# Kernel optimization log

Measured on AMD Instinct MI355X. Metric: run time of the kernel, lower is better.

The kernel has to match this reference:

```python
import jax, jax.numpy as jnp
import numpy as np

NUM_HEADS = 32
KV_HEADS = 8
HEAD_DIM = 128
HIDDEN = 4096
Q_DIM = NUM_HEADS * HEAD_DIM      # 4096
KV_DIM = KV_HEADS * HEAD_DIM      # 1024
GROUP = NUM_HEADS // KV_HEADS     # 4 (GQA)
ROPE_THETA = 10000.0
LORA_SCALE = 0.5
BP, S = 4, 1024                   # prefill requests x prefill seq len
BD, L = 64, 2048                  # decode requests x cached kv len
R, NA = 16, 8                     # lora rank, num adapters


def _rope(x, pos):
    # x: [..., n_heads, HEAD_DIM]; pos broadcastable over the token dims of x
    half = x.shape[-1] // 2
    inv = 1.0 / (ROPE_THETA ** (jnp.arange(half, dtype=jnp.float32) / half))
    freqs = pos[..., None].astype(jnp.float32) * inv          # pos.shape + (half,)
    cos = jnp.cos(freqs)[..., None, :]                        # insert head axis
    sin = jnp.sin(freqs)[..., None, :]
    x1, x2 = x[..., :half], x[..., half:]
    return jnp.concatenate([x1 * cos - x2 * sin, x2 * cos + x1 * sin], axis=-1)


def _lora(x, A, B, idx):
    # grouped multi-adapter LoRA: per-request adapter selection
    # x: [b, ..., H]; A: [NA, H, R]; B: [NA, R, D]; idx: [b]
    t = jnp.einsum('b...h,bhr->b...r', x, A[idx])
    return LORA_SCALE * jnp.einsum('b...r,brd->b...d', t, B[idx])


def setup_inputs() -> dict:
    key = jax.random.key(0)
    ks = jax.random.split(key, 16)
    T = BP * S + BD
    w = lambda k, shp: (jax.random.normal(k, shp, jnp.float32) * 0.02)
    return {
        'hidden_states': jax.random.normal(ks[0], (T, HIDDEN), jnp.float32),
        'w_qkv': w(ks[1], (HIDDEN, Q_DIM + 2 * KV_DIM)),
        'w_o': w(ks[2], (Q_DIM, HIDDEN)),
        'k_cache': jax.random.normal(ks[3], (BD, L, KV_HEADS, HEAD_DIM), jnp.float32),
        'v_cache': jax.random.normal(ks[4], (BD, L, KV_HEADS, HEAD_DIM), jnp.float32),
        'lora_a_q': w(ks[5], (NA, HIDDEN, R)),
        'lora_b_q': w(ks[6], (NA, R, Q_DIM)),
        'lora_a_k': w(ks[7], (NA, HIDDEN, R)),
        'lora_b_k': w(ks[8], (NA, R, KV_DIM)),
        'lora_a_v': w(ks[9], (NA, HIDDEN, R)),
        'lora_b_v': w(ks[10], (NA, R, KV_DIM)),
        'lora_a_o': w(ks[11], (NA, Q_DIM, R)),
        'lora_b_o': w(ks[12], (NA, R, HIDDEN)),
        'prefill_adapter_idx': jax.random.randint(ks[13], (BP,), 0, NA),
        'decode_adapter_idx': jax.random.randint(ks[14], (BD,), 0, NA),
    }


def reference(hidden_states, w_qkv, w_o, k_cache, v_cache,
              lora_a_q, lora_b_q, lora_a_k, lora_b_k, lora_a_v, lora_b_v,
              lora_a_o, lora_b_o, prefill_adapter_idx, decode_adapter_idx):
    TP = BP * S
    qkv = hidden_states @ w_qkv
    q, k, v = jnp.split(qkv, [Q_DIM, Q_DIM + KV_DIM], axis=1)

    x_p = hidden_states[:TP].reshape(BP, S, HIDDEN)
    x_d = hidden_states[TP:]

    # apply_lora_weight_kvq: per-request adapters on q/k/v
    q_p = q[:TP].reshape(BP, S, Q_DIM) + _lora(x_p, lora_a_q, lora_b_q, prefill_adapter_idx)
    k_p = k[:TP].reshape(BP, S, KV_DIM) + _lora(x_p, lora_a_k, lora_b_k, prefill_adapter_idx)
    v_p = v[:TP].reshape(BP, S, KV_DIM) + _lora(x_p, lora_a_v, lora_b_v, prefill_adapter_idx)
    q_d = q[TP:] + _lora(x_d, lora_a_q, lora_b_q, decode_adapter_idx)
    k_d = k[TP:] + _lora(x_d, lora_a_k, lora_b_k, decode_adapter_idx)
    v_d = v[TP:] + _lora(x_d, lora_a_v, lora_b_v, decode_adapter_idx)

    scale = 1.0 / np.sqrt(HEAD_DIM).astype(np.float32)

    # ---- prefill: causal self-attention with on-the-fly RoPE ----
    q_p = _rope(q_p.reshape(BP, S, NUM_HEADS, HEAD_DIM), jnp.arange(S, dtype=jnp.float32))
    k_p = _rope(k_p.reshape(BP, S, KV_HEADS, HEAD_DIM), jnp.arange(S, dtype=jnp.float32))
    v_p = v_p.reshape(BP, S, KV_HEADS, HEAD_DIM)
    kr = jnp.repeat(k_p, GROUP, axis=2)
    vr = jnp.repeat(v_p, GROUP, axis=2)
    scores = jnp.einsum('bqhd,bkhd->bhqk', q_p, kr) * scale
    causal = jnp.tril(jnp.ones((S, S), bool))
    scores = jnp.where(causal, scores, -jnp.inf)
    attn = jax.nn.softmax(scores, axis=-1)
    out_p = jnp.einsum('bhqk,bkhd->bqhd', attn, vr).reshape(TP, Q_DIM)

    # ---- decode: one new token per request vs paged KV cache ----
    q_d = _rope(q_d.reshape(BD, NUM_HEADS, HEAD_DIM), jnp.asarray(L, jnp.float32))
    k_new = _rope(k_d.reshape(BD, KV_HEADS, HEAD_DIM), jnp.asarray(L, jnp.float32))
    k_hist = _rope(k_cache, jnp.arange(L, dtype=jnp.float32))
    k_all = jnp.concatenate([k_hist, k_new[:, None]], axis=1)   # [BD, L+1, kvh, hd]
    v_all = jnp.concatenate([v_cache, v_d.reshape(BD, 1, KV_HEADS, HEAD_DIM)], axis=1)
    kr2 = jnp.repeat(k_all, GROUP, axis=2)
    vr2 = jnp.repeat(v_all, GROUP, axis=2)
    s2 = jnp.einsum('bhd,bkhd->bhk', q_d, kr2) * scale
    a2 = jax.nn.softmax(s2, axis=-1)
    out_d = jnp.einsum('bhk,bkhd->bhd', a2, vr2).reshape(BD, Q_DIM)

    # ---- o_proj + apply_lora_weight_attn ----
    attn_raw = jnp.concatenate([out_p, out_d], axis=0)
    o = attn_raw @ w_o
    o_p = o[:TP].reshape(BP, S, HIDDEN) + _lora(attn_raw[:TP].reshape(BP, S, Q_DIM), lora_a_o, lora_b_o, prefill_adapter_idx)
    o_d = o[TP:] + _lora(attn_raw[TP:], lora_a_o, lora_b_o, decode_adapter_idx)
    return jnp.concatenate([o_p.reshape(TP, HIDDEN), o_d], axis=0)
```

## Files before the change

### kernel.cpp

```cpp
#include <hip/hip_runtime.h>

#define NUM_HEADS 32
#define KV_HEADS 8
#define HEAD_DIM 128
#define HIDDEN 4096
#define Q_DIM 4096
#define KV_DIM 1024
#define QKV_DIM 6144
#define GROUP 4
#define BP 4
#define S_LEN 1024
#define BD 64
#define L_CTX 2048
#define RANK 16
#define NA 8
#define TP (BP * S_LEN)
#define T_TOT (TP + BD)
#define M_PAD 4224
#define SCALE 0.08838834764831845f
#define LORA_SCALE 0.5f
#define DNSPLIT 16
#define DSPLIT_LEN 128
#define DP_STRIDE 520

typedef float fv4 __attribute__((ext_vector_type(4)));
typedef __bf16 bf16x8 __attribute__((ext_vector_type(8)));
typedef unsigned short usv4 __attribute__((ext_vector_type(4)));
typedef unsigned short u16;

__device__ __forceinline__ float b2f(u16 u) {
    unsigned int x = ((unsigned int)u) << 16;
    return __builtin_bit_cast(float, x);
}
__device__ __forceinline__ u16 f2b(float f) {
    unsigned int u = __builtin_bit_cast(unsigned int, f);
    unsigned int r = u + 0x7fffu + ((u >> 16) & 1u);
    return (u16)(r >> 16);
}
__device__ __forceinline__ void gload_lds16(const void* g, void* l) {
    __builtin_amdgcn_global_load_lds((const __attribute__((address_space(1))) void*)g,
                                     (__attribute__((address_space(3))) void*)l, 16, 0, 0);
}
__device__ __forceinline__ float dot16(const float* __restrict__ a, const float* __restrict__ b) {
    float s = 0.f;
#pragma unroll
    for (int q = 0; q < 4; ++q) {
        fv4 av = *(const fv4*)(a + q * 4);
        fv4 bv = *(const fv4*)(b + q * 4);
        s += av[0] * bv[0] + av[1] * bv[1] + av[2] * bv[2] + av[3] * bv[3];
    }
    return s;
}

#define OFF_QKV  ((size_t)0)
#define OFF_ATTN OFF_QKV
#define OFF_HB   ((size_t)51904512)
#define OFF_QP   OFF_HB
#define OFF_WOT  OFF_HB
#define OFF_WQT  ((size_t)86507520)
#define OFF_KP   ((size_t)86507520)
#define OFF_VP   ((size_t)94896128)
#define OFF_QD   ((size_t)103284736)
#define OFF_KD   ((size_t)104333312)
#define OFF_VD   ((size_t)104595456)
#define OFF_DP   ((size_t)104857600)
#define OFF_BQT  ((size_t)121896960)
#define OFF_BKT  ((size_t)123994112)
#define OFF_BVT  ((size_t)124518400)
#define OFF_BOT  ((size_t)125042688)
#define OFF_T    ((size_t)136839168)
#define OFF_TO   ((size_t)137637888)
#define OFF_COS  ((size_t)137904128)
#define OFF_SIN  ((size_t)138428672)

__global__ void rope_tab_kernel(float* ctab, float* stab) {
    int idx = blockIdx.x * 256 + threadIdx.x;
    if (idx >= 2049 * 64) return;
    int pos = idx >> 6, d = idx & 63;
    float inv = 1.0f / powf(10000.0f, (float)d / 64.0f);
    float f = (float)pos * inv;
    ctab[idx] = cosf(f);
    stab[idx] = sinf(f);
}

__global__ void conv_hidden_kernel(const float* __restrict__ x, u16* __restrict__ y) {
    int gid = blockIdx.x * 256 + threadIdx.x;
    if (gid >= M_PAD * (HIDDEN / 8)) return;
    size_t base = (size_t)gid * 8;
    int row = gid >> 9;
    usv4 lo, hi;
    if (row < T_TOT) {
        fv4 a = *(const fv4*)(x + base);
        fv4 b = *(const fv4*)(x + base + 4);
        lo[0] = f2b(a[0]); lo[1] = f2b(a[1]); lo[2] = f2b(a[2]); lo[3] = f2b(a[3]);
        hi[0] = f2b(b[0]); hi[1] = f2b(b[1]); hi[2] = f2b(b[2]); hi[3] = f2b(b[3]);
    } else {
        lo[0] = 0; lo[1] = 0; lo[2] = 0; lo[3] = 0;
        hi[0] = 0; hi[1] = 0; hi[2] = 0; hi[3] = 0;
    }
    *(usv4*)(y + base) = lo;
    *(usv4*)(y + base + 4) = hi;
}

__global__ __launch_bounds__(256) void transpose_f32_bf16_kernel(const float* __restrict__ in,
                                                                 u16* __restrict__ out,
                                                                 int R, int C) {
    __shared__ float tile[64][65];
    int r0 = blockIdx.y * 64, c0 = blockIdx.x * 64;
    int t = threadIdx.x;
    int tr = t >> 4, tc4 = (t & 15) * 4;
#pragma unroll
    for (int it = 0; it < 4; ++it) {
        int r = tr + it * 16;
        fv4 v = *(const fv4*)(in + (size_t)(r0 + r) * C + c0 + tc4);
        tile[r][tc4 + 0] = v[0]; tile[r][tc4 + 1] = v[1];
        tile[r][tc4 + 2] = v[2]; tile[r][tc4 + 3] = v[3];
    }
    __syncthreads();
#pragma unroll
    for (int it = 0; it < 4; ++it) {
        int c = tr + it * 16;
        usv4 st;
        st[0] = f2b(tile[tc4 + 0][c]); st[1] = f2b(tile[tc4 + 1][c]);
        st[2] = f2b(tile[tc4 + 2][c]); st[3] = f2b(tile[tc4 + 3][c]);
        *(usv4*)(out + (size_t)(c0 + c) * R + r0 + tc4) = st;
    }
}

__global__ void btrans_kernel(const float* __restrict__ Bq, const float* __restrict__ Bk,
                              const float* __restrict__ Bv, const float* __restrict__ Bo,
                              float* __restrict__ BqT, float* __restrict__ BkT,
                              float* __restrict__ BvT, float* __restrict__ BoT) {
    int gid = blockIdx.x * 256 + threadIdx.x;
    const int NQ = NA * 4096 * 16;
    const int NK = NA * 1024 * 16;
    if (gid < NQ) {
        int a = gid >> 16, rem = gid & 65535, c = rem >> 4, r = rem & 15;
        BqT[gid] = Bq[((size_t)(a * 16 + r)) * 4096 + c];
    } else if (gid < NQ + NK) {
        int g = gid - NQ;
        int a = g >> 14, rem = g & 16383, c = rem >> 4, r = rem & 15;
        BkT[g] = Bk[((size_t)(a * 16 + r)) * 1024 + c];
    } else if (gid < NQ + 2 * NK) {
        int g = gid - NQ - NK;
        int a = g >> 14, rem = g & 16383, c = rem >> 4, r = rem & 15;
        BvT[g] = Bv[((size_t)(a * 16 + r)) * 1024 + c];
    } else if (gid < 2 * NQ + 2 * NK) {
        int g = gid - NQ - 2 * NK;
        int a = g >> 16, rem = g & 65535, c = rem >> 4, r = rem & 15;
        BoT[g] = Bo[((size_t)(a * 16 + r)) * 4096 + c];
    }
}

__global__ __launch_bounds__(256) void lora_a_kernel(const float* __restrict__ x,
                              const float* __restrict__ Aq, const float* __restrict__ Ak,
                              const float* __restrict__ Av,
                              const int* __restrict__ pidx, const int* __restrict__ didx,
                              float* __restrict__ T) {
    __shared__ float xs[4][HIDDEN];
    int t0 = blockIdx.x * 4;
    int tid = threadIdx.x;
    for (int j = tid; j < 4096; j += 256) {
        int tok = j >> 10, off = (j & 1023) * 4;
        *(fv4*)&xs[tok][off] = *(const fv4*)(x + (size_t)(t0 + tok) * HIDDEN + off);
    }
    __syncthreads();
    int w = tid >> 6, lane = tid & 63;
    if (w >= 3) return;
    const float* Ab = (w == 0) ? Aq : (w == 1 ? Ak : Av);
    float acc[4][16];
#pragma unroll
    for (int tk = 0; tk < 4; ++tk)
#pragma unroll
        for (int r = 0; r < 16; ++r) acc[tk][r] = 0.f;
#pragma unroll
    for (int tk = 0; tk < 4; ++tk) {
        int t = t0 + tk;
        int a = (t < TP) ? pidx[t >> 10] : didx[t - TP];
        const float* A = Ab + (size_t)a * HIDDEN * RANK;
        for (int i = 0; i < 64; ++i) {
            int hh = i * 64 + lane;
            float xv = xs[tk][hh];
            const float* Ar = A + (size_t)hh * RANK;
            fv4 a0 = *(const fv4*)Ar, a1 = *(const fv4*)(Ar + 4);
            fv4 a2 = *(const fv4*)(Ar + 8), a3 = *(const fv4*)(Ar + 12);
#pragma unroll
            for (int r = 0; r < 4; ++r) {
                acc[tk][r] += xv * a0[r];
                acc[tk][4 + r] += xv * a1[r];
                acc[tk][8 + r] += xv * a2[r];
                acc[tk][12 + r] += xv * a3[r];
            }
        }
    }
#pragma unroll
    for (int tk = 0; tk < 4; ++tk)
#pragma unroll
        for (int r = 0; r < 16; ++r) {
            float v = acc[tk][r];
            v += __shfl_xor(v, 1); v += __shfl_xor(v, 2); v += __shfl_xor(v, 4);
            v += __shfl_xor(v, 8); v += __shfl_xor(v, 16); v += __shfl_xor(v, 32);
            if (lane == r) T[(size_t)(t0 + tk) * 48 + w * 16 + r] = v;
        }
}

template <int OUT_BF16>
__global__ __launch_bounds__(256) void gemm_bt_kernel(const u16* __restrict__ A,
                                                      const u16* __restrict__ BT,
                                                      void* __restrict__ Cp,
                                                      int Mstore, int N, int K) {
    __shared__ __align__(16) u16 As[2][128 * 32];
    __shared__ __align__(16) u16 Bs[2][128 * 32];
    int tid = threadIdx.x;
    int m0 = blockIdx.y * 128, n0 = blockIdx.x * 128;
    int lane = tid & 63, w = tid >> 6, lr = lane & 15, lg = lane >> 4;
    int wr = w >> 1, wc = w & 1;
    int arow = tid >> 2, acol = (tid & 3) * 8;
    const u16* Ab = A + (size_t)(m0 + arow) * K + acol;
    const u16* Bb = BT + (size_t)(n0 + arow) * K + acol;
    fv4 acc[4][4] = {};
    int nt = K / 32;
#define GSTAGE(buf, kk)                                                             \
    {                                                                               \
        char* Ad = (char*)&As[buf][0] + w * 1024;                                   \
        char* Bd = (char*)&Bs[buf][0] + w * 1024;                                   \
        gload_lds16(Ab + (kk), Ad);                                                 \
        gload_lds16(Ab + (size_t)64 * K + (kk), Ad + 4096);                         \
        gload_lds16(Bb + (kk), Bd);                                                 \
        gload_lds16(Bb + (size_t)64 * K + (kk), Bd + 4096);                         \
    }
    GSTAGE(0, 0)
    __syncthreads();
    int cur = 0;
    for (int t = 0; t < nt; ++t) {
        if (t + 1 < nt) GSTAGE(cur ^ 1, (t + 1) * 32)
        bf16x8 af[4], bf[4];
#pragma unroll
        for (int i = 0; i < 4; ++i) {
            af[i] = *(const bf16x8*)&As[cur][(wr * 64 + i * 16 + lr) * 32 + lg * 8];
            bf[i] = *(const bf16x8*)&Bs[cur][(wc * 64 + i * 16 + lr) * 32 + lg * 8];
        }
#pragma unroll
        for (int mi = 0; mi < 4; ++mi)
#pragma unroll
            for (int ni = 0; ni < 4; ++ni)
                acc[mi][ni] = __builtin_amdgcn_mfma_f32_16x16x32_bf16(af[mi], bf[ni], acc[mi][ni], 0, 0, 0);
        __syncthreads();
        cur ^= 1;
    }
#undef GSTAGE
#pragma unroll
    for (int mi = 0; mi < 4; ++mi)
#pragma unroll
        for (int ni = 0; ni < 4; ++ni) {
            int col = n0 + wc * 64 + ni * 16 + lr;
#pragma unroll
            for (int r = 0; r < 4; ++r) {
                int row = m0 + wr * 64 + mi * 16 + lg * 4 + r;
                if (row < Mstore) {
                    if (OUT_BF16)
                        ((u16*)Cp)[(size_t)row * N + col] = f2b(acc[mi][ni][r]);
                    else
                        ((float*)Cp)[(size_t)row * N + col] = acc[mi][ni][r];
                }
            }
        }
}

__global__ __launch_bounds__(256) void lorab_rope_scatter_kernel(
    const u16* __restrict__ qkv, const float* __restrict__ T,
    const float* __restrict__ BqT, const float* __restrict__ BkT, const float* __restrict__ BvT,
    const int* __restrict__ pidx, const int* __restrict__ didx,
    const float* __restrict__ ctab, const float* __restrict__ stab,
    u16* __restrict__ qp, u16* __restrict__ kp, u16* __restrict__ vp,
    float* __restrict__ qd, float* __restrict__ kd, float* __restrict__ vd) {
    int t = blockIdx.x;
    __shared__ __align__(16) float Ts[48];
    if (threadIdx.x < 48) Ts[threadIdx.x] = T[(size_t)t * 48 + threadIdx.x];
    __syncthreads();
    bool pre = t < TP;
    int a = pre ? pidx[t >> 10] : didx[t - TP];
    int pos = pre ? (t & 1023) : L_CTX;
    int b = t >> 10;
    int td = t - TP;
    const u16* qrow = qkv + (size_t)t * QKV_DIM;
    for (int p = threadIdx.x; p < 3072; p += 256) {
        if (p < 2048) {
            int h = p >> 6, d = p & 63;
            int col = h * 128 + d;
            float v1 = b2f(qrow[col]), v2 = b2f(qrow[col + 64]);
            const float* B1 = BqT + ((size_t)(a * 4096 + col)) * 16;
            const float* B2 = BqT + ((size_t)(a * 4096 + col + 64)) * 16;
            float l1 = dot16(&Ts[0], B1);
            float l2 = dot16(&Ts[0], B2);
            v1 += LORA_SCALE * l1; v2 += LORA_SCALE * l2;
            float c = ctab[pos * 64 + d], s = stab[pos * 64 + d];
            float o1 = v1 * c - v2 * s, o2 = v2 * c + v1 * s;
            if (pre) {
                size_t base = (((size_t)(b * 32 + h)) * 1024 + pos) * 128 + d;
                qp[base] = f2b(o1); qp[base + 64] = f2b(o2);
            } else {
                size_t base = ((size_t)(td * 32 + h)) * 128 + d;
                qd[base] = o1; qd[base + 64] = o2;
            }
        } else if (p < 2560) {
            int pp = p - 2048;
            int h = pp >> 6, d = pp & 63;
            int jc = h * 128 + d;
            int col = Q_DIM + jc;
            float v1 = b2f(qrow[col]), v2 = b2f(qrow[col + 64]);
            const float* B1 = BkT + ((size_t)(a * 1024 + jc)) * 16;
            const float* B2 = BkT + ((size_t)(a * 1024 + jc + 64)) * 16;
            float l1 = dot16(&Ts[16], B1);
            float l2 = dot16(&Ts[16], B2);
            v1 += LORA_SCALE * l1; v2 += LORA_SCALE * l2;
            float c = ctab[pos * 64 + d], s = stab[pos * 64 + d];
            float o1 = v1 * c - v2 * s, o2 = v2 * c + v1 * s;
            if (pre) {
                size_t base = (((size_t)(b * 8 + h)) * 1024 + pos) * 128 + d;
                kp[base] = f2b(o1); kp[base + 64] = f2b(o2);
            } else {
                size_t base = ((size_t)(td * 8 + h)) * 128 + d;
                kd[base] = o1; kd[base + 64] = o2;
            }
        } else {
            int pp = p - 2560;
            int h = pp >> 6, d = pp & 63;
            int jc = h * 128 + d;
            int col = Q_DIM + KV_DIM + jc;
            float v1 = b2f(qrow[col]), v2 = b2f(qrow[col + 64]);
            const float* B1 = BvT + ((size_t)(a * 1024 + jc)) * 16;
            const float* B2 = BvT + ((size_t)(a * 1024 + jc + 64)) * 16;
            float l1 = dot16(&Ts[32], B1);
            float l2 = dot16(&Ts[32], B2);
            v1 += LORA_SCALE * l1; v2 += LORA_SCALE * l2;
            if (pre) {
                size_t base = (((size_t)(b * 8 + h)) * 1024 + pos) * 128 + d;
                vp[base] = f2b(v1); vp[base + 64] = f2b(v2);
            } else {
                size_t base = ((size_t)(td * 8 + h)) * 128 + d;
                vd[base] = v1; vd[base + 64] = v2;
            }
        }
    }
}

__global__ __launch_bounds__(256) void prefill_attn_kernel(const u16* __restrict__ qp,
                                                           const u16* __restrict__ kp,
                                                           const u16* __restrict__ vp,
                                                           u16* __restrict__ attn) {
    int bx = blockIdx.x;
    int qt = (bx & 1) ? (31 - (bx >> 1)) : (bx >> 1);
    int kvh = blockIdx.y, b = blockIdx.z;
    int tid = threadIdx.x, w = tid >> 6, lane = tid & 63, lr = lane & 15, lg = lane >> 4;
    int h = kvh * 4 + w;
    const u16* Q = qp + ((size_t)(b * 32 + h)) * 1024 * 128;
    const u16* K = kp + ((size_t)(b * 8 + kvh)) * 1024 * 128;
    const u16* V = vp + ((size_t)(b * 8 + kvh)) * 1024 * 128;
    int qc0 = qt * 32 + lr, qc1 = qt * 32 + 16 + lr;
    bf16x8 qf0[4], qf1[4];
#pragma unroll
    for (int dc = 0; dc < 4; ++dc) {
        qf0[dc] = *(const bf16x8*)(Q + (size_t)qc0 * 128 + dc * 32 + lg * 8);
        qf1[dc] = *(const bf16x8*)(Q + (size_t)qc1 * 128 + dc * 32 + lg * 8);
    }
    fv4 o0[8] = {}, o1[8] = {};
    float m0 = -INFINITY, l0 = 0.f;
    float m1 = -INFINITY, l1 = 0.f;
    int nkb = qt + 1;
    for (int kb = 0; kb < nkb; ++kb) {
        int k0 = kb * 32;
        fv4 s00 = {}, s10 = {}, s01 = {}, s11 = {};
#pragma unroll
        for (int dc = 0; dc < 4; ++dc) {
            bf16x8 kf0 = *(const bf16x8*)(K + (size_t)(k0 + lr) * 128 + dc * 32 + lg * 8);
            bf16x8 kf1 = *(const bf16x8*)(K + (size_t)(k0 + 16 + lr) * 128 + dc * 32 + lg * 8);
            s00 = __builtin_amdgcn_mfma_f32_16x16x32_bf16(kf0, qf0[dc], s00, 0, 0, 0);
            s10 = __builtin_amdgcn_mfma_f32_16x16x32_bf16(kf1, qf0[dc], s10, 0, 0, 0);
            s01 = __builtin_amdgcn_mfma_f32_16x16x32_bf16(kf0, qf1[dc], s01, 0, 0, 0);
            s11 = __builtin_amdgcn_mfma_f32_16x16x32_bf16(kf1, qf1[dc], s11, 0, 0, 0);
        }
        bf16x8 vf[8];
#pragma unroll
        for (int c = 0; c < 8; ++c)
#pragma unroll
            for (int i = 0; i < 4; ++i) {
                vf[c][i] = __builtin_bit_cast(__bf16, V[(size_t)(k0 + lg * 4 + i) * 128 + c * 16 + lr]);
                vf[c][4 + i] = __builtin_bit_cast(__bf16, V[(size_t)(k0 + 16 + lg * 4 + i) * 128 + c * 16 + lr]);
            }
        bf16x8 pf0, pf1;
        {
            float p0[4], p1[4];
            float lm = -INFINITY;
#pragma unroll
            for (int r = 0; r < 4; ++r) {
                float x = s00[r] * SCALE;
                if (k0 + lg * 4 + r > qc0) x = -INFINITY;
                p0[r] = x; lm = fmaxf(lm, x);
                x = s10[r] * SCALE;
                if (k0 + 16 + lg * 4 + r > qc0) x = -INFINITY;
                p1[r] = x; lm = fmaxf(lm, x);
            }
            lm = fmaxf(lm, __shfl_xor(lm, 16));
            lm = fmaxf(lm, __shfl_xor(lm, 32));
            float mn = fmaxf(m0, lm);
            float sc = __expf(m0 - mn);
            float rs = 0.f;
#pragma unroll
            for (int r = 0; r < 4; ++r) {
                p0[r] = __expf(p0[r] - mn);
                p1[r] = __expf(p1[r] - mn);
                rs += p0[r] + p1[r];
            }
            rs += __shfl_xor(rs, 16);
            rs += __shfl_xor(rs, 32);
            l0 = l0 * sc + rs;
            m0 = mn;
#pragma unroll
            for (int c = 0; c < 8; ++c) o0[c] *= sc;
#pragma unroll
            for (int r = 0; r < 4; ++r) {
                pf0[r] = (__bf16)p0[r];
                pf0[4 + r] = (__bf16)p1[r];
            }
        }
        {
            float p0[4], p1[4];
            float lm = -INFINITY;
#pragma unroll
            for (int r = 0; r < 4; ++r) {
                float x = s01[r] * SCALE;
                if (k0 + lg * 4 + r > qc1) x = -INFINITY;
                p0[r] = x; lm = fmaxf(lm, x);
                x = s11[r] * SCALE;
                if (k0 + 16 + lg * 4 + r > qc1) x = -INFINITY;
                p1[r] = x; lm = fmaxf(lm, x);
            }
            lm = fmaxf(lm, __shfl_xor(lm, 16));
            lm = fmaxf(lm, __shfl_xor(lm, 32));
            float mn = fmaxf(m1, lm);
            float sc = __expf(m1 - mn);
            float rs = 0.f;
#pragma unroll
            for (int r = 0; r < 4; ++r) {
                p0[r] = __expf(p0[r] - mn);
                p1[r] = __expf(p1[r] - mn);
                rs += p0[r] + p1[r];
            }
            rs += __shfl_xor(rs, 16);
            rs += __shfl_xor(rs, 32);
            l1 = l1 * sc + rs;
            m1 = mn;
#pragma unroll
            for (int c = 0; c < 8; ++c) o1[c] *= sc;
#pragma unroll
            for (int r = 0; r < 4; ++r) {
                pf1[r] = (__bf16)p0[r];
                pf1[4 + r] = (__bf16)p1[r];
            }
        }
#pragma unroll
        for (int c = 0; c < 8; ++c) {
            o0[c] = __builtin_amdgcn_mfma_f32_16x16x32_bf16(vf[c], pf0, o0[c], 0, 0, 0);
            o1[c] = __builtin_amdgcn_mfma_f32_16x16x32_bf16(vf[c], pf1, o1[c], 0, 0, 0);
        }
    }
    float inv0 = 1.0f / l0, inv1 = 1.0f / l1;
    size_t trow0 = (size_t)(b * 1024 + qc0) * Q_DIM;
    size_t trow1 = (size_t)(b * 1024 + qc1) * Q_DIM;
#pragma unroll
    for (int c = 0; c < 8; ++c)
#pragma unroll
        for (int r = 0; r < 4; ++r) {
            int feat = h * 128 + c * 16 + lg * 4 + r;
            attn[trow0 + feat] = f2b(o0[c][r] * inv0);
            attn[trow1 + feat] = f2b(o1[c][r] * inv1);
        }
}

template <int FIRST_HALF>
__device__ __forceinline__ bf16x8 krope8(const float* __restrict__ Krow,
                                         const float* __restrict__ ct,
                                         const float* __restrict__ st, int d0) {
    bf16x8 out;
    if (FIRST_HALF) {
        fv4 a0 = *(const fv4*)(Krow + d0), a1 = *(const fv4*)(Krow + d0 + 4);
        fv4 b0 = *(const fv4*)(Krow + d0 + 64), b1 = *(const fv4*)(Krow + d0 + 68);
        fv4 c0 = *(const fv4*)(ct + d0), c1 = *(const fv4*)(ct + d0 + 4);
        fv4 s0 = *(const fv4*)(st + d0), s1 = *(const fv4*)(st + d0 + 4);
#pragma unroll
        for (int i = 0; i < 4; ++i) {
            out[i] = (__bf16)(a0[i] * c0[i] - b0[i] * s0[i]);
            out[4 + i] = (__bf16)(a1[i] * c1[i] - b1[i] * s1[i]);
        }
    } else {
        int dd = d0 - 64;
        fv4 a0 = *(const fv4*)(Krow + d0), a1 = *(const fv4*)(Krow + d0 + 4);
        fv4 b0 = *(const fv4*)(Krow + dd), b1 = *(const fv4*)(Krow + dd + 4);
        fv4 c0 = *(const fv4*)(ct + dd), c1 = *(const fv4*)(ct + dd + 4);
        fv4 s0 = *(const fv4*)(st + dd), s1 = *(const fv4*)(st + dd + 4);
#pragma unroll
        for (int i = 0; i < 4; ++i) {
            out[i] = (__bf16)(a0[i] * c0[i] + b0[i] * s0[i]);
            out[4 + i] = (__bf16)(a1[i] * c1[i] + b1[i] * s1[i]);
        }
    }
    return out;
}

__global__ __launch_bounds__(128) void decode_attn_kernel(const float* __restrict__ kc,
                                                          const float* __restrict__ vc,
                                                          const float* __restrict__ qd,
                                                          const float* __restrict__ ctab,
                                                          const float* __restrict__ stab,
                                                          float* __restrict__ dp) {
    int blk = blockIdx.x;
    int bk = blk >> 3;
    int b = bk >> 3, kvh = bk & 7;
    int wv = threadIdx.x >> 6, lane = threadIdx.x & 63;
    int s = (blk & 7) * 2 + wv;
    int lr = lane & 15, lg = lane >> 4;
    const float* Qrow = qd + ((size_t)(b * 32 + kvh * 4 + (lr & 3))) * 128;
    bf16x8 qf[4];
#pragma unroll
    for (int dc = 0; dc < 4; ++dc) {
        int d0 = dc * 32 + lg * 8;
        fv4 q0 = *(const fv4*)(Qrow + d0), q1 = *(const fv4*)(Qrow + d0 + 4);
#pragma unroll
        for (int i = 0; i < 4; ++i) {
            qf[dc][i] = (__bf16)q0[i];
            qf[dc][4 + i] = (__bf16)q1[i];
        }
    }
    fv4 o[8] = {};
    float m = -INFINITY, l = 0.f;
    int kbase = s * DSPLIT_LEN;
    for (int t = 0; t < 4; ++t) {
        int k0 = kbase + t * 32;
        int key0 = k0 + lr, key1 = k0 + 16 + lr;
        const float* K0 = kc + (((size_t)b * L_CTX + key0) * 8 + kvh) * 128;
        const float* K1 = kc + (((size_t)b * L_CTX + key1) * 8 + kvh) * 128;
        const float* ct0 = ctab + key0 * 64;
        const float* st0 = stab + key0 * 64;
        const float* ct1 = ctab + key1 * 64;
        const float* st1 = stab + key1 * 64;
        fv4 s0 = {}, s1 = {};
#pragma unroll
        for (int dc = 0; dc < 4; ++dc) {
            int d0 = dc * 32 + lg * 8;
            bf16x8 kf0, kf1;
            if (dc < 2) {
                kf0 = krope8<1>(K0, ct0, st0, d0);
                kf1 = krope8<1>(K1, ct1, st1, d0);
            } else {
                kf0 = krope8<0>(K0, ct0, st0, d0);
                kf1 = krope8<0>(K1, ct1, st1, d0);
            }
            s0 = __builtin_amdgcn_mfma_f32_16x16x32_bf16(kf0, qf[dc], s0, 0, 0, 0);
            s1 = __builtin_amdgcn_mfma_f32_16x16x32_bf16(kf1, qf[dc], s1, 0, 0, 0);
        }
        const float* Vb = vc + (((size_t)b * L_CTX + k0) * 8 + kvh) * 128;
        bf16x8 vf[8];
#pragma unroll
        for (int c = 0; c < 8; ++c)
#pragma unroll
            for (int i = 0; i < 4; ++i) {
                vf[c][i] = (__bf16)Vb[(size_t)(lg * 4 + i) * 1024 + c * 16 + lr];
                vf[c][4 + i] = (__bf16)Vb[(size_t)(16 + lg * 4 + i) * 1024 + c * 16 + lr];
            }
        float p0[4], p1[4];
        float lm = -INFINITY;
#pragma unroll
        for (int r = 0; r < 4; ++r) {
            float x = s0[r] * SCALE;
            p0[r] = x; lm = fmaxf(lm, x);
            x = s1[r] * SCALE;
            p1[r] = x; lm = fmaxf(lm, x);
        }
        lm = fmaxf(lm, __shfl_xor(lm, 16));
        lm = fmaxf(lm, __shfl_xor(lm, 32));
        float mn = fmaxf(m, lm);
        float sc = __expf(m - mn);
        float rs = 0.f;
#pragma unroll
        for (int r = 0; r < 4; ++r) {
            p0[r] = __expf(p0[r] - mn);
            p1[r] = __expf(p1[r] - mn);
            rs += p0[r] + p1[r];
        }
        rs += __shfl_xor(rs, 16);
        rs += __shfl_xor(rs, 32);
        l = l * sc + rs;
        m = mn;
#pragma unroll
        for (int c = 0; c < 8; ++c) o[c] *= sc;
        bf16x8 pf;
#pragma unroll
        for (int r = 0; r < 4; ++r) {
            pf[r] = (__bf16)p0[r];
            pf[4 + r] = (__bf16)p1[r];
        }
#pragma unroll
        for (int c = 0; c < 8; ++c)
            o[c] = __builtin_amdgcn_mfma_f32_16x16x32_bf16(vf[c], pf, o[c], 0, 0, 0);
    }
    size_t base = ((size_t)(bk * DNSPLIT + s)) * DP_STRIDE;
    if (lr < 4) {
#pragma unroll
        for (int c = 0; c < 8; ++c)
#pragma unroll
            for (int r = 0; r < 4; ++r)
                dp[base + 8 + lr * 128 + c * 16 + lg * 4 + r] = o[c][r];
        if (lg == 0) { dp[base + lr] = m; dp[base + 4 + lr] = l; }
    }
}

__global__ __launch_bounds__(256) void decode_merge_kernel(const float* __restrict__ dp,
                                                           const float* __restrict__ qd,
                                                           const float* __restrict__ kd,
                                                           const float* __restrict__ vd,
                                                           u16* __restrict__ attn) {
    int bk = blockIdx.x;
    int b = bk >> 3, kvh = bk & 7;
    int g = threadIdx.x >> 6, lane = threadIdx.x & 63;
    size_t qb = ((size_t)(b * 32 + kvh * 4 + g)) * 128;
    float q1 = qd[qb + lane], q2 = qd[qb + 64 + lane];
    size_t kb = ((size_t)(b * 8 + kvh)) * 128;
    float k1 = kd[kb + lane], k2 = kd[kb + 64 + lane];
    float v1 = vd[kb + lane], v2 = vd[kb + 64 + lane];
    float part = q1 * k1 + q2 * k2;
#pragma unroll
    for (int off = 32; off; off >>= 1) part += __shfl_xor(part, off);
    float snew = part * SCALE;
    float M = snew;
#pragma unroll
    for (int s = 0; s < DNSPLIT; ++s)
        M = fmaxf(M, dp[((size_t)(bk * DNSPLIT + s)) * DP_STRIDE + g]);
    float L = 0.f, O1 = 0.f, O2 = 0.f;
#pragma unroll
    for (int s = 0; s < DNSPLIT; ++s) {
        size_t base = ((size_t)(bk * DNSPLIT + s)) * DP_STRIDE;
        float e = __expf(dp[base + g] - M);
        L += dp[base + 4 + g] * e;
        O1 += dp[base + 8 + g * 128 + lane] * e;
        O2 += dp[base + 8 + g * 128 + 64 + lane] * e;
    }
    float en = __expf(snew - M);
    L += en; O1 += en * v1; O2 += en * v2;
    size_t orow = (size_t)(TP + b) * Q_DIM + (kvh * 4 + g) * 128;
    attn[orow + lane] = f2b(O1 / L);
    attn[orow + 64 + lane] = f2b(O2 / L);
}

__global__ __launch_bounds__(64) void lora_o_a_kernel(const u16* __restrict__ attn,
                                const float* __restrict__ Ao,
                                const int* __restrict__ pidx, const int* __restrict__ didx,
                                float* __restrict__ To) {
    __shared__ float xs[4][HIDDEN];
    int t0 = blockIdx.x * 4;
    int lane = threadIdx.x;
    for (int j = lane; j < 4096; j += 64) {
        int tok = j >> 10, off = (j & 1023) * 4;
        usv4 v = *(const usv4*)(attn + (size_t)(t0 + tok) * Q_DIM + off);
        xs[tok][off] = b2f(v[0]); xs[tok][off + 1] = b2f(v[1]);
        xs[tok][off + 2] = b2f(v[2]); xs[tok][off + 3] = b2f(v[3]);
    }
    __syncthreads();
    float acc[4][16];
#pragma unroll
    for (int tk = 0; tk < 4; ++tk)
#pragma unroll
        for (int r = 0; r < 16; ++r) acc[tk][r] = 0.f;
#pragma unroll
    for (int tk = 0; tk < 4; ++tk) {
        int t = t0 + tk;
        int a = (t < TP) ? pidx[t >> 10] : didx[t - TP];
        const float* A = Ao + (size_t)a * Q_DIM * RANK;
        for (int i = 0; i < 64; ++i) {
            int hh = i * 64 + lane;
            float xv = xs[tk][hh];
            const float* Ar = A + (size_t)hh * RANK;
            fv4 a0 = *(const fv4*)Ar, a1 = *(const fv4*)(Ar + 4);
            fv4 a2 = *(const fv4*)(Ar + 8), a3 = *(const fv4*)(Ar + 12);
#pragma unroll
            for (int r = 0; r < 4; ++r) {
                acc[tk][r] += xv * a0[r];
                acc[tk][4 + r] += xv * a1[r];
                acc[tk][8 + r] += xv * a2[r];
                acc[tk][12 + r] += xv * a3[r];
            }
        }
    }
#pragma unroll
    for (int tk = 0; tk < 4; ++tk)
#pragma unroll
        for (int r = 0; r < 16; ++r) {
            float v = acc[tk][r];
            v += __shfl_xor(v, 1); v += __shfl_xor(v, 2); v += __shfl_xor(v, 4);
            v += __shfl_xor(v, 8); v += __shfl_xor(v, 16); v += __shfl_xor(v, 32);
            if (lane == r) To[(size_t)(t0 + tk) * RANK + r] = v;
        }
}

__global__ void final_lora_add_kernel(float* __restrict__ out, const float* __restrict__ To,
                                      const float* __restrict__ BoT,
                                      const int* __restrict__ pidx, const int* __restrict__ didx) {
    int gid = blockIdx.x * 256 + threadIdx.x;
    if (gid >= T_TOT * HIDDEN) return;
    int t = gid >> 12, j = gid & 4095;
    int a = (t < TP) ? pidx[t >> 10] : didx[t - TP];
    const float* B = BoT + ((size_t)(a * 4096 + j)) * 16;
    const float* Tr = To + (size_t)t * RANK;
    out[gid] += LORA_SCALE * dot16(Tr, B);
}

extern "C" void kernel_launch(void* const* d_in, const int* in_sizes, int n_in,
                              void* d_out, int out_size, void* d_ws, size_t ws_size,
                              hipStream_t stream) {
    const float* hidden = (const float*)d_in[0];
    const float* w_qkv = (const float*)d_in[1];
    const float* w_o = (const float*)d_in[2];
    const float* k_cache = (const float*)d_in[3];
    const float* v_cache = (const float*)d_in[4];
    const float* Aq = (const float*)d_in[5];
    const float* Bq = (const float*)d_in[6];
    const float* Ak = (const float*)d_in[7];
    const float* Bk = (const float*)d_in[8];
    const float* Av = (const float*)d_in[9];
    const float* Bv = (const float*)d_in[10];
    const float* Ao = (const float*)d_in[11];
    const float* Bo = (const float*)d_in[12];
    const int* pidx = (const int*)d_in[13];
    const int* didx = (const int*)d_in[14];
    float* out = (float*)d_out;

    char* ws = (char*)d_ws;
    u16* qkv = (u16*)(ws + OFF_QKV);
    u16* attn = (u16*)(ws + OFF_ATTN);
    u16* hb = (u16*)(ws + OFF_HB);
    u16* wqT = (u16*)(ws + OFF_WQT);
    u16* woT = (u16*)(ws + OFF_WOT);
    float* T = (float*)(ws + OFF_T);
    u16* qp = (u16*)(ws + OFF_QP);
    u16* kp = (u16*)(ws + OFF_KP);
    u16* vp = (u16*)(ws + OFF_VP);
    float* qd = (float*)(ws + OFF_QD);
    float* kd = (float*)(ws + OFF_KD);
    float* vd = (float*)(ws + OFF_VD);
    float* dp = (float*)(ws + OFF_DP);
    float* BqT = (float*)(ws + OFF_BQT);
    float* BkT = (float*)(ws + OFF_BKT);
    float* BvT = (float*)(ws + OFF_BVT);
    float* BoT = (float*)(ws + OFF_BOT);
    float* To = (float*)(ws + OFF_TO);
    float* ctab = (float*)(ws + OFF_COS);
    float* stab = (float*)(ws + OFF_SIN);

    rope_tab_kernel<<<513, 256, 0, stream>>>(ctab, stab);
    conv_hidden_kernel<<<(M_PAD * (HIDDEN / 8) + 255) / 256, 256, 0, stream>>>(hidden, hb);
    transpose_f32_bf16_kernel<<<dim3(QKV_DIM / 64, HIDDEN / 64), 256, 0, stream>>>(w_qkv, wqT, HIDDEN, QKV_DIM);
    lora_a_kernel<<<T_TOT / 4, 256, 0, stream>>>(hidden, Aq, Ak, Av, pidx, didx, T);
    gemm_bt_kernel<1><<<dim3(QKV_DIM / 128, M_PAD / 128), 256, 0, stream>>>(hb, wqT, qkv, M_PAD, QKV_DIM, HIDDEN);
    btrans_kernel<<<(2 * (NA * 4096 * 16) + 2 * (NA * 1024 * 16) + 255) / 256, 256, 0, stream>>>(
        Bq, Bk, Bv, Bo, BqT, BkT, BvT, BoT);
    lorab_rope_scatter_kernel<<<T_TOT, 256, 0, stream>>>(qkv, T, BqT, BkT, BvT, pidx, didx,
                                                         ctab, stab, qp, kp, vp, qd, kd, vd);
    prefill_attn_kernel<<<dim3(32, 8, 4), 256, 0, stream>>>(qp, kp, vp, attn);
    decode_attn_kernel<<<4096, 128, 0, stream>>>(k_cache, v_cache, qd, ctab, stab, dp);
    decode_merge_kernel<<<512, 256, 0, stream>>>(dp, qd, kd, vd, attn);
    transpose_f32_bf16_kernel<<<dim3(HIDDEN / 64, Q_DIM / 64), 256, 0, stream>>>(w_o, woT, Q_DIM, HIDDEN);
    lora_o_a_kernel<<<T_TOT / 4, 64, 0, stream>>>(attn, Ao, pidx, didx, To);
    gemm_bt_kernel<0><<<dim3(HIDDEN / 128, M_PAD / 128), 256, 0, stream>>>(attn, woT, out, T_TOT, HIDDEN, Q_DIM);
    final_lora_add_kernel<<<(T_TOT * HIDDEN + 255) / 256, 256, 0, stream>>>(out, To, BoT, pidx, didx);
}
```

Before: 1.633 ms.

## Fuse prefill and decode attention into one interleaved launch

Merges the prefill flash-attention kernel and the split-K decode attention kernel into a single launch of 3072 blocks. Every third block runs a prefill tile and the other two run decode splits, with decode blocks now holding 4 waves instead of 2. The aim is to overlap the memory-bound decode KV-cache streaming with the compute-heavy causal prefill and remove one launch plus its tail. The cost is higher register pressure from the union of both paths, which may lower occupancy, and a block-role branch.

New measurement: 1.695 ms. +3.8%, slower.

```diff
diff --git a/kernel.cpp b/kernel.cpp
--- a/kernel.cpp
+++ b/kernel.cpp
@@ -345,139 +345,6 @@
     }
 }
 
-__global__ __launch_bounds__(256) void prefill_attn_kernel(const u16* __restrict__ qp,
-                                                           const u16* __restrict__ kp,
-                                                           const u16* __restrict__ vp,
-                                                           u16* __restrict__ attn) {
-    int bx = blockIdx.x;
-    int qt = (bx & 1) ? (31 - (bx >> 1)) : (bx >> 1);
-    int kvh = blockIdx.y, b = blockIdx.z;
-    int tid = threadIdx.x, w = tid >> 6, lane = tid & 63, lr = lane & 15, lg = lane >> 4;
-    int h = kvh * 4 + w;
-    const u16* Q = qp + ((size_t)(b * 32 + h)) * 1024 * 128;
-    const u16* K = kp + ((size_t)(b * 8 + kvh)) * 1024 * 128;
-    const u16* V = vp + ((size_t)(b * 8 + kvh)) * 1024 * 128;
-    int qc0 = qt * 32 + lr, qc1 = qt * 32 + 16 + lr;
-    bf16x8 qf0[4], qf1[4];
-#pragma unroll
-    for (int dc = 0; dc < 4; ++dc) {
-        qf0[dc] = *(const bf16x8*)(Q + (size_t)qc0 * 128 + dc * 32 + lg * 8);
-        qf1[dc] = *(const bf16x8*)(Q + (size_t)qc1 * 128 + dc * 32 + lg * 8);
-    }
-    fv4 o0[8] = {}, o1[8] = {};
-    float m0 = -INFINITY, l0 = 0.f;
-    float m1 = -INFINITY, l1 = 0.f;
-    int nkb = qt + 1;
-    for (int kb = 0; kb < nkb; ++kb) {
-        int k0 = kb * 32;
-        fv4 s00 = {}, s10 = {}, s01 = {}, s11 = {};
-#pragma unroll
-        for (int dc = 0; dc < 4; ++dc) {
-            bf16x8 kf0 = *(const bf16x8*)(K + (size_t)(k0 + lr) * 128 + dc * 32 + lg * 8);
-            bf16x8 kf1 = *(const bf16x8*)(K + (size_t)(k0 + 16 + lr) * 128 + dc * 32 + lg * 8);
-            s00 = __builtin_amdgcn_mfma_f32_16x16x32_bf16(kf0, qf0[dc], s00, 0, 0, 0);
-            s10 = __builtin_amdgcn_mfma_f32_16x16x32_bf16(kf1, qf0[dc], s10, 0, 0, 0);
-            s01 = __builtin_amdgcn_mfma_f32_16x16x32_bf16(kf0, qf1[dc], s01, 0, 0, 0);
-            s11 = __builtin_amdgcn_mfma_f32_16x16x32_bf16(kf1, qf1[dc], s11, 0, 0, 0);
-        }
-        bf16x8 vf[8];
-#pragma unroll
-        for (int c = 0; c < 8; ++c)
-#pragma unroll
-            for (int i = 0; i < 4; ++i) {
-                vf[c][i] = __builtin_bit_cast(__bf16, V[(size_t)(k0 + lg * 4 + i) * 128 + c * 16 + lr]);
-                vf[c][4 + i] = __builtin_bit_cast(__bf16, V[(size_t)(k0 + 16 + lg * 4 + i) * 128 + c * 16 + lr]);
-            }
-        bf16x8 pf0, pf1;
-        {
-            float p0[4], p1[4];
-            float lm = -INFINITY;
-#pragma unroll
-            for (int r = 0; r < 4; ++r) {
-                float x = s00[r] * SCALE;
-                if (k0 + lg * 4 + r > qc0) x = -INFINITY;
-                p0[r] = x; lm = fmaxf(lm, x);
-                x = s10[r] * SCALE;
-                if (k0 + 16 + lg * 4 + r > qc0) x = -INFINITY;
-                p1[r] = x; lm = fmaxf(lm, x);
-            }
-            lm = fmaxf(lm, __shfl_xor(lm, 16));
-            lm = fmaxf(lm, __shfl_xor(lm, 32));
-            float mn = fmaxf(m0, lm);
-            float sc = __expf(m0 - mn);
-            float rs = 0.f;
-#pragma unroll
-            for (int r = 0; r < 4; ++r) {
-                p0[r] = __expf(p0[r] - mn);
-                p1[r] = __expf(p1[r] - mn);
-                rs += p0[r] + p1[r];
-            }
-            rs += __shfl_xor(rs, 16);
-            rs += __shfl_xor(rs, 32);
-            l0 = l0 * sc + rs;
-            m0 = mn;
-#pragma unroll
-            for (int c = 0; c < 8; ++c) o0[c] *= sc;
-#pragma unroll
-            for (int r = 0; r < 4; ++r) {
-                pf0[r] = (__bf16)p0[r];
-                pf0[4 + r] = (__bf16)p1[r];
-            }
-        }
-        {
-            float p0[4], p1[4];
-            float lm = -INFINITY;
-#pragma unroll
-            for (int r = 0; r < 4; ++r) {
-                float x = s01[r] * SCALE;
-                if (k0 + lg * 4 + r > qc1) x = -INFINITY;
-                p0[r] = x; lm = fmaxf(lm, x);
-                x = s11[r] * SCALE;
-                if (k0 + 16 + lg * 4 + r > qc1) x = -INFINITY;
-                p1[r] = x; lm = fmaxf(lm, x);
-            }
-            lm = fmaxf(lm, __shfl_xor(lm, 16));
-            lm = fmaxf(lm, __shfl_xor(lm, 32));
-            float mn = fmaxf(m1, lm);
-            float sc = __expf(m1 - mn);
-            float rs = 0.f;
-#pragma unroll
-            for (int r = 0; r < 4; ++r) {
-                p0[r] = __expf(p0[r] - mn);
-                p1[r] = __expf(p1[r] - mn);
-                rs += p0[r] + p1[r];
-            }
-            rs += __shfl_xor(rs, 16);
-            rs += __shfl_xor(rs, 32);
-            l1 = l1 * sc + rs;
-            m1 = mn;
-#pragma unroll
-            for (int c = 0; c < 8; ++c) o1[c] *= sc;
-#pragma unroll
-            for (int r = 0; r < 4; ++r) {
-                pf1[r] = (__bf16)p0[r];
-                pf1[4 + r] = (__bf16)p1[r];
-            }
-        }
-#pragma unroll
-        for (int c = 0; c < 8; ++c) {
-            o0[c] = __builtin_amdgcn_mfma_f32_16x16x32_bf16(vf[c], pf0, o0[c], 0, 0, 0);
-            o1[c] = __builtin_amdgcn_mfma_f32_16x16x32_bf16(vf[c], pf1, o1[c], 0, 0, 0);
-        }
-    }
-    float inv0 = 1.0f / l0, inv1 = 1.0f / l1;
-    size_t trow0 = (size_t)(b * 1024 + qc0) * Q_DIM;
-    size_t trow1 = (size_t)(b * 1024 + qc1) * Q_DIM;
-#pragma unroll
-    for (int c = 0; c < 8; ++c)
-#pragma unroll
-        for (int r = 0; r < 4; ++r) {
-            int feat = h * 128 + c * 16 + lg * 4 + r;
-            attn[trow0 + feat] = f2b(o0[c][r] * inv0);
-            attn[trow1 + feat] = f2b(o1[c][r] * inv1);
-        }
-}
-
 template <int FIRST_HALF>
 __device__ __forceinline__ bf16x8 krope8(const float* __restrict__ Krow,
                                          const float* __restrict__ ct,
@@ -508,110 +375,240 @@
     return out;
 }
 
-__global__ __launch_bounds__(128) void decode_attn_kernel(const float* __restrict__ kc,
-                                                          const float* __restrict__ vc,
-                                                          const float* __restrict__ qd,
-                                                          const float* __restrict__ ctab,
-                                                          const float* __restrict__ stab,
-                                                          float* __restrict__ dp) {
-    int blk = blockIdx.x;
-    int bk = blk >> 3;
-    int b = bk >> 3, kvh = bk & 7;
-    int wv = threadIdx.x >> 6, lane = threadIdx.x & 63;
-    int s = (blk & 7) * 2 + wv;
-    int lr = lane & 15, lg = lane >> 4;
-    const float* Qrow = qd + ((size_t)(b * 32 + kvh * 4 + (lr & 3))) * 128;
-    bf16x8 qf[4];
-#pragma unroll
-    for (int dc = 0; dc < 4; ++dc) {
-        int d0 = dc * 32 + lg * 8;
-        fv4 q0 = *(const fv4*)(Qrow + d0), q1 = *(const fv4*)(Qrow + d0 + 4);
-#pragma unroll
-        for (int i = 0; i < 4; ++i) {
-            qf[dc][i] = (__bf16)q0[i];
-            qf[dc][4 + i] = (__bf16)q1[i];
-        }
-    }
-    fv4 o[8] = {};
-    float m = -INFINITY, l = 0.f;
-    int kbase = s * DSPLIT_LEN;
-    for (int t = 0; t < 4; ++t) {
-        int k0 = kbase + t * 32;
-        int key0 = k0 + lr, key1 = k0 + 16 + lr;
-        const float* K0 = kc + (((size_t)b * L_CTX + key0) * 8 + kvh) * 128;
-        const float* K1 = kc + (((size_t)b * L_CTX + key1) * 8 + kvh) * 128;
-        const float* ct0 = ctab + key0 * 64;
-        const float* st0 = stab + key0 * 64;
-        const float* ct1 = ctab + key1 * 64;
-        const float* st1 = stab + key1 * 64;
-        fv4 s0 = {}, s1 = {};
+__global__ __launch_bounds__(256) void attn_fused_kernel(
+    const u16* __restrict__ qp, const u16* __restrict__ kp, const u16* __restrict__ vp,
+    u16* __restrict__ attn,
+    const float* __restrict__ kc, const float* __restrict__ vc, const float* __restrict__ qd,
+    const float* __restrict__ ctab, const float* __restrict__ stab, float* __restrict__ dp) {
+    int bid = blockIdx.x;
+    int tid = threadIdx.x, lane = tid & 63, lr = lane & 15, lg = lane >> 4;
+    if (bid % 3 == 0) {
+        int pb = bid / 3;
+        int bx = pb & 31, kvh = (pb >> 5) & 7, b = pb >> 8;
+        int qt = (bx & 1) ? (31 - (bx >> 1)) : (bx >> 1);
+        int w = tid >> 6;
+        int h = kvh * 4 + w;
+        const u16* Q = qp + ((size_t)(b * 32 + h)) * 1024 * 128;
+        const u16* K = kp + ((size_t)(b * 8 + kvh)) * 1024 * 128;
+        const u16* V = vp + ((size_t)(b * 8 + kvh)) * 1024 * 128;
+        int qc0 = qt * 32 + lr, qc1 = qt * 32 + 16 + lr;
+        bf16x8 qf0[4], qf1[4];
+#pragma unroll
+        for (int dc = 0; dc < 4; ++dc) {
+            qf0[dc] = *(const bf16x8*)(Q + (size_t)qc0 * 128 + dc * 32 + lg * 8);
+            qf1[dc] = *(const bf16x8*)(Q + (size_t)qc1 * 128 + dc * 32 + lg * 8);
+        }
+        fv4 o0[8] = {}, o1[8] = {};
+        float m0 = -INFINITY, l0 = 0.f;
+        float m1 = -INFINITY, l1 = 0.f;
+        int nkb = qt + 1;
+        for (int kb = 0; kb < nkb; ++kb) {
+            int k0 = kb * 32;
+            fv4 s00 = {}, s10 = {}, s01 = {}, s11 = {};
+#pragma unroll
+            for (int dc = 0; dc < 4; ++dc) {
+                bf16x8 kf0 = *(const bf16x8*)(K + (size_t)(k0 + lr) * 128 + dc * 32 + lg * 8);
+                bf16x8 kf1 = *(const bf16x8*)(K + (size_t)(k0 + 16 + lr) * 128 + dc * 32 + lg * 8);
+                s00 = __builtin_amdgcn_mfma_f32_16x16x32_bf16(kf0, qf0[dc], s00, 0, 0, 0);
+                s10 = __builtin_amdgcn_mfma_f32_16x16x32_bf16(kf1, qf0[dc], s10, 0, 0, 0);
+                s01 = __builtin_amdgcn_mfma_f32_16x16x32_bf16(kf0, qf1[dc], s01, 0, 0, 0);
+                s11 = __builtin_amdgcn_mfma_f32_16x16x32_bf16(kf1, qf1[dc], s11, 0, 0, 0);
+            }
+            bf16x8 vf[8];
+#pragma unroll
+            for (int c = 0; c < 8; ++c)
+#pragma unroll
+                for (int i = 0; i < 4; ++i) {
+                    vf[c][i] = __builtin_bit_cast(__bf16, V[(size_t)(k0 + lg * 4 + i) * 128 + c * 16 + lr]);
+                    vf[c][4 + i] = __builtin_bit_cast(__bf16, V[(size_t)(k0 + 16 + lg * 4 + i) * 128 + c * 16 + lr]);
+                }
+            bf16x8 pf0, pf1;
+            {
+                float p0[4], p1[4];
+                float lm = -INFINITY;
+#pragma unroll
+                for (int r = 0; r < 4; ++r) {
+                    float x = s00[r] * SCALE;
+                    if (k0 + lg * 4 + r > qc0) x = -INFINITY;
+                    p0[r] = x; lm = fmaxf(lm, x);
+                    x = s10[r] * SCALE;
+                    if (k0 + 16 + lg * 4 + r > qc0) x = -INFINITY;
+                    p1[r] = x; lm = fmaxf(lm, x);
+                }
+                lm = fmaxf(lm, __shfl_xor(lm, 16));
+                lm = fmaxf(lm, __shfl_xor(lm, 32));
+                float mn = fmaxf(m0, lm);
+                float sc = __expf(m0 - mn);
+                float rs = 0.f;
+#pragma unroll
+                for (int r = 0; r < 4; ++r) {
+                    p0[r] = __expf(p0[r] - mn);
+                    p1[r] = __expf(p1[r] - mn);
+                    rs += p0[r] + p1[r];
+                }
+                rs += __shfl_xor(rs, 16);
+                rs += __shfl_xor(rs, 32);
+                l0 = l0 * sc + rs;
+                m0 = mn;
+#pragma unroll
+                for (int c = 0; c < 8; ++c) o0[c] *= sc;
+#pragma unroll
+                for (int r = 0; r < 4; ++r) {
+                    pf0[r] = (__bf16)p0[r];
+                    pf0[4 + r] = (__bf16)p1[r];
+                }
+            }
+            {
+                float p0[4], p1[4];
+                float lm = -INFINITY;
+#pragma unroll
+                for (int r = 0; r < 4; ++r) {
+                    float x = s01[r] * SCALE;
+                    if (k0 + lg * 4 + r > qc1) x = -INFINITY;
+                    p0[r] = x; lm = fmaxf(lm, x);
+                    x = s11[r] * SCALE;
+                    if (k0 + 16 + lg * 4 + r > qc1) x = -INFINITY;
+                    p1[r] = x; lm = fmaxf(lm, x);
+                }
+                lm = fmaxf(lm, __shfl_xor(lm, 16));
+                lm = fmaxf(lm, __shfl_xor(lm, 32));
+                float mn = fmaxf(m1, lm);
+                float sc = __expf(m1 - mn);
+                float rs = 0.f;
+#pragma unroll
+                for (int r = 0; r < 4; ++r) {
+                    p0[r] = __expf(p0[r] - mn);
+                    p1[r] = __expf(p1[r] - mn);
+                    rs += p0[r] + p1[r];
+                }
+                rs += __shfl_xor(rs, 16);
+                rs += __shfl_xor(rs, 32);
+                l1 = l1 * sc + rs;
+                m1 = mn;
+#pragma unroll
+                for (int c = 0; c < 8; ++c) o1[c] *= sc;
+#pragma unroll
+                for (int r = 0; r < 4; ++r) {
+                    pf1[r] = (__bf16)p0[r];
+                    pf1[4 + r] = (__bf16)p1[r];
+                }
+            }
+#pragma unroll
+            for (int c = 0; c < 8; ++c) {
+                o0[c] = __builtin_amdgcn_mfma_f32_16x16x32_bf16(vf[c], pf0, o0[c], 0, 0, 0);
+                o1[c] = __builtin_amdgcn_mfma_f32_16x16x32_bf16(vf[c], pf1, o1[c], 0, 0, 0);
+            }
+        }
+        float inv0 = 1.0f / l0, inv1 = 1.0f / l1;
+        size_t trow0 = (size_t)(b * 1024 + qc0) * Q_DIM;
+        size_t trow1 = (size_t)(b * 1024 + qc1) * Q_DIM;
+#pragma unroll
+        for (int c = 0; c < 8; ++c)
+#pragma unroll
+            for (int r = 0; r < 4; ++r) {
+                int feat = h * 128 + c * 16 + lg * 4 + r;
+                attn[trow0 + feat] = f2b(o0[c][r] * inv0);
+                attn[trow1 + feat] = f2b(o1[c][r] * inv1);
+            }
+    } else {
+        int db = (bid / 3) * 2 + (bid % 3) - 1;
+        int bk = db >> 2;
+        int b = bk >> 3, kvh = bk & 7;
+        int wv = tid >> 6;
+        int s = (db & 3) * 4 + wv;
+        const float* Qrow = qd + ((size_t)(b * 32 + kvh * 4 + (lr & 3))) * 128;
+        bf16x8 qf[4];
 #pragma unroll
         for (int dc = 0; dc < 4; ++dc) {
             int d0 = dc * 32 + lg * 8;
-            bf16x8 kf0, kf1;
-            if (dc < 2) {
-                kf0 = krope8<1>(K0, ct0, st0, d0);
-                kf1 = krope8<1>(K1, ct1, st1, d0);
-            } else {
-                kf0 = krope8<0>(K0, ct0, st0, d0);
-                kf1 = krope8<0>(K1, ct1, st1, d0);
-            }
-            s0 = __builtin_amdgcn_mfma_f32_16x16x32_bf16(kf0, qf[dc], s0, 0, 0, 0);
-            s1 = __builtin_amdgcn_mfma_f32_16x16x32_bf16(kf1, qf[dc], s1, 0, 0, 0);
-        }
-        const float* Vb = vc + (((size_t)b * L_CTX + k0) * 8 + kvh) * 128;
-        bf16x8 vf[8];
-#pragma unroll
-        for (int c = 0; c < 8; ++c)
+            fv4 q0 = *(const fv4*)(Qrow + d0), q1 = *(const fv4*)(Qrow + d0 + 4);
 #pragma unroll
             for (int i = 0; i < 4; ++i) {
-                vf[c][i] = (__bf16)Vb[(size_t)(lg * 4 + i) * 1024 + c * 16 + lr];
-                vf[c][4 + i] = (__bf16)Vb[(size_t)(16 + lg * 4 + i) * 1024 + c * 16 + lr];
-            }
-        float p0[4], p1[4];
-        float lm = -INFINITY;
-#pragma unroll
-        for (int r = 0; r < 4; ++r) {
-            float x = s0[r] * SCALE;
-            p0[r] = x; lm = fmaxf(lm, x);
-            x = s1[r] * SCALE;
-            p1[r] = x; lm = fmaxf(lm, x);
-        }
-        lm = fmaxf(lm, __shfl_xor(lm, 16));
-        lm = fmaxf(lm, __shfl_xor(lm, 32));
-        float mn = fmaxf(m, lm);
-        float sc = __expf(m - mn);
-        float rs = 0.f;
-#pragma unroll
-        for (int r = 0; r < 4; ++r) {
-            p0[r] = __expf(p0[r] - mn);
-            p1[r] = __expf(p1[r] - mn);
-            rs += p0[r] + p1[r];
-        }
-        rs += __shfl_xor(rs, 16);
-        rs += __shfl_xor(rs, 32);
-        l = l * sc + rs;
-        m = mn;
-#pragma unroll
-        for (int c = 0; c < 8; ++c) o[c] *= sc;
-        bf16x8 pf;
-#pragma unroll
-        for (int r = 0; r < 4; ++r) {
-            pf[r] = (__bf16)p0[r];
-            pf[4 + r] = (__bf16)p1[r];
-        }
-#pragma unroll
-        for (int c = 0; c < 8; ++c)
-            o[c] = __builtin_amdgcn_mfma_f32_16x16x32_bf16(vf[c], pf, o[c], 0, 0, 0);
-    }
-    size_t base = ((size_t)(bk * DNSPLIT + s)) * DP_STRIDE;
-    if (lr < 4) {
-#pragma unroll
-        for (int c = 0; c < 8; ++c)
-#pragma unroll
-            for (int r = 0; r < 4; ++r)
-                dp[base + 8 + lr * 128 + c * 16 + lg * 4 + r] = o[c][r];
-        if (lg == 0) { dp[base + lr] = m; dp[base + 4 + lr] = l; }
+                qf[dc][i] = (__bf16)q0[i];
+                qf[dc][4 + i] = (__bf16)q1[i];
+            }
+        }
+        fv4 o[8] = {};
+        float m = -INFINITY, l = 0.f;
+        int kbase = s * DSPLIT_LEN;
+        for (int t = 0; t < 4; ++t) {
+            int k0 = kbase + t * 32;
+            int key0 = k0 + lr, key1 = k0 + 16 + lr;
+            const float* K0 = kc + (((size_t)b * L_CTX + key0) * 8 + kvh) * 128;
+            const float* K1 = kc + (((size_t)b * L_CTX + key1) * 8 + kvh) * 128;
+            const float* ct0 = ctab + key0 * 64;
+            const float* st0 = stab + key0 * 64;
+            const float* ct1 = ctab + key1 * 64;
+            const float* st1 = stab + key1 * 64;
+            fv4 s0 = {}, s1 = {};
+#pragma unroll
+            for (int dc = 0; dc < 4; ++dc) {
+                int d0 = dc * 32 + lg * 8;
+                bf16x8 kf0, kf1;
+                if (dc < 2) {
+                    kf0 = krope8<1>(K0, ct0, st0, d0);
+                    kf1 = krope8<1>(K1, ct1, st1, d0);
+                } else {
+                    kf0 = krope8<0>(K0, ct0, st0, d0);
+                    kf1 = krope8<0>(K1, ct1, st1, d0);
+                }
+                s0 = __builtin_amdgcn_mfma_f32_16x16x32_bf16(kf0, qf[dc], s0, 0, 0, 0);
+                s1 = __builtin_amdgcn_mfma_f32_16x16x32_bf16(kf1, qf[dc], s1, 0, 0, 0);
+            }
+            const float* Vb = vc + (((size_t)b * L_CTX + k0) * 8 + kvh) * 128;
+            bf16x8 vf[8];
+#pragma unroll
+            for (int c = 0; c < 8; ++c)
+#pragma unroll
+                for (int i = 0; i < 4; ++i) {
+                    vf[c][i] = (__bf16)Vb[(size_t)(lg * 4 + i) * 1024 + c * 16 + lr];
+                    vf[c][4 + i] = (__bf16)Vb[(size_t)(16 + lg * 4 + i) * 1024 + c * 16 + lr];
+                }
+            float p0[4], p1[4];
+            float lm = -INFINITY;
+#pragma unroll
+            for (int r = 0; r < 4; ++r) {
+                float x = s0[r] * SCALE;
+                p0[r] = x; lm = fmaxf(lm, x);
+                x = s1[r] * SCALE;
+                p1[r] = x; lm = fmaxf(lm, x);
+            }
+            lm = fmaxf(lm, __shfl_xor(lm, 16));
+            lm = fmaxf(lm, __shfl_xor(lm, 32));
+            float mn = fmaxf(m, lm);
+            float sc = __expf(m - mn);
+            float rs = 0.f;
+#pragma unroll
+            for (int r = 0; r < 4; ++r) {
+                p0[r] = __expf(p0[r] - mn);
+                p1[r] = __expf(p1[r] - mn);
+                rs += p0[r] + p1[r];
+            }
+            rs += __shfl_xor(rs, 16);
+            rs += __shfl_xor(rs, 32);
+            l = l * sc + rs;
+            m = mn;
+#pragma unroll
+            for (int c = 0; c < 8; ++c) o[c] *= sc;
+            bf16x8 pf;
+#pragma unroll
+            for (int r = 0; r < 4; ++r) {
+                pf[r] = (__bf16)p0[r];
+                pf[4 + r] = (__bf16)p1[r];
+            }
+#pragma unroll
+            for (int c = 0; c < 8; ++c)
+                o[c] = __builtin_amdgcn_mfma_f32_16x16x32_bf16(vf[c], pf, o[c], 0, 0, 0);
+        }
+        size_t base = ((size_t)(bk * DNSPLIT + s)) * DP_STRIDE;
+        if (lr < 4) {
+#pragma unroll
+            for (int c = 0; c < 8; ++c)
+#pragma unroll
+                for (int r = 0; r < 4; ++r)
+                    dp[base + 8 + lr * 128 + c * 16 + lg * 4 + r] = o[c][r];
+            if (lg == 0) { dp[base + lr] = m; dp[base + 4 + lr] = l; }
+        }
     }
 }
 
@@ -765,8 +762,7 @@
         Bq, Bk, Bv, Bo, BqT, BkT, BvT, BoT);
     lorab_rope_scatter_kernel<<<T_TOT, 256, 0, stream>>>(qkv, T, BqT, BkT, BvT, pidx, didx,
                                                          ctab, stab, qp, kp, vp, qd, kd, vd);
-    prefill_attn_kernel<<<dim3(32, 8, 4), 256, 0, stream>>>(qp, kp, vp, attn);
-    decode_attn_kernel<<<4096, 128, 0, stream>>>(k_cache, v_cache, qd, ctab, stab, dp);
+    attn_fused_kernel<<<3072, 256, 0, stream>>>(qp, kp, vp, attn, k_cache, v_cache, qd, ctab, stab, dp);
     decode_merge_kernel<<<512, 256, 0, stream>>>(dp, qd, kd, vd, attn);
     transpose_f32_bf16_kernel<<<dim3(HIDDEN / 64, Q_DIM / 64), 256, 0, stream>>>(w_o, woT, Q_DIM, HIDDEN);
     lora_o_a_kernel<<<T_TOT / 4, 64, 0, stream>>>(attn, Ao, pidx, didx, To);
```
